# Kernel tuning notes

Measured on AMD Instinct MI355X. Metric: run time of the kernel, lower is better.

The kernel has to match this reference:

```python
import jax, jax.numpy as jnp
import numpy as np
import math

B, T, E, H = 2, 2048, 1024, 16
D = E // H  # head_dim = 64


def setup_inputs() -> dict:
    key = jax.random.key(0)
    ks = jax.random.split(key, 8)
    s = 1.0 / math.sqrt(E)
    x = jax.random.normal(ks[0], (B, T, E), dtype=jnp.float32)
    # Linear weights stored as [in, out] so y = x @ W (equivalent to torch x @ W.T)
    Wq = jax.random.normal(ks[1], (E, E), dtype=jnp.float32) * s
    Wk = jax.random.normal(ks[2], (E, E), dtype=jnp.float32) * s
    Wv = jax.random.normal(ks[3], (E, E), dtype=jnp.float32) * s
    Wa = jax.random.normal(ks[4], (E, H), dtype=jnp.float32) * s
    Wg = jax.random.normal(ks[5], (E, E), dtype=jnp.float32) * s
    Wo = jax.random.normal(ks[6], (E, E), dtype=jnp.float32) * s
    A_log = jnp.linspace(0.0, math.log(16.0), H, dtype=jnp.float32)
    dt_bias = jnp.zeros((H,), dtype=jnp.float32)
    rms_w = jnp.ones((D,), dtype=jnp.float32)
    return {"x": x, "Wq": Wq, "Wk": Wk, "Wv": Wv, "Wa": Wa, "Wg": Wg,
            "Wo": Wo, "A_log": A_log, "dt_bias": dt_bias, "rms_w": rms_w}


def _l2norm(t):
    n = jnp.linalg.norm(t, axis=-1, keepdims=True)
    return t / jnp.maximum(n, 1e-12)


def reference(x, Wq, Wk, Wv, Wa, Wg, Wo, A_log, dt_bias, rms_w):
    b, seq_len, e = x.shape
    h = A_log.shape[0]
    d = e // h
    # QKV projections, L2-normalize q and k over head_dim -> [b, h, t, d]
    q = _l2norm((x @ Wq).reshape(b, seq_len, h, d)).transpose(0, 2, 1, 3)
    k = _l2norm((x @ Wk).reshape(b, seq_len, h, d)).transpose(0, 2, 1, 3)
    v = (x @ Wv).reshape(b, seq_len, h, d).transpose(0, 2, 1, 3)
    # scalar decay alpha in (0,1]: exp(-exp(A_log) * softplus(x @ Wa + dt_bias))
    dt = jax.nn.softplus(x @ Wa + dt_bias)           # [b, t, h]
    alpha = jnp.exp(-jnp.exp(A_log) * dt)            # [b, t, h]
    # decay mask L_ij = prod_{s=j+1}^{i} alpha_s (i >= j), via cumulative log-sum
    cum_log = jnp.cumsum(jnp.log(alpha + 1e-8), axis=1).transpose(0, 2, 1)  # [b, h, t]
    log_l = cum_log[..., :, None] - cum_log[..., None, :]                   # [b, h, t, t]
    causal = jnp.tril(jnp.ones((seq_len, seq_len), dtype=bool))
    l_mat = jnp.where(causal, jnp.exp(log_l), 0.0)
    # quadratic form: Y = (L * Q K^T) V
    scores = jnp.einsum('bhid,bhjd->bhij', q, k) * l_mat
    out = jnp.einsum('bhij,bhjd->bhid', scores, v)   # [b, h, t, d]
    # RMSNorm over head_dim (eps=1e-6)
    out = out * jax.lax.rsqrt(jnp.mean(out * out, axis=-1, keepdims=True) + 1e-6) * rms_w
    out = out.transpose(0, 2, 1, 3).reshape(b, seq_len, e)
    gate = jax.nn.silu(x @ Wg)
    return (out * gate) @ Wo
```

## Files before the change

### kernel.cpp

```cpp
#include <hip/hip_runtime.h>
#include <hip/hip_bf16.h>
#include <math.h>

#define B_ 2
#define T_ 2048
#define E_ 1024
#define H_ 16
#define D_ 64
#define MTOK (B_*T_)

typedef __bf16 bf16;
typedef __bf16 bf16x8 __attribute__((ext_vector_type(8)));
typedef __bf16 bf16x4 __attribute__((ext_vector_type(4)));
typedef float  f32x4  __attribute__((ext_vector_type(4)));

__device__ __forceinline__ void gl_lds16(const void* g, void* l) {
    __builtin_amdgcn_global_load_lds(
        (const __attribute__((address_space(1))) void*)g,
        (__attribute__((address_space(3))) void*)l, 16, 0, 0);
}

__global__ void prep_weights_kernel(const float* __restrict__ Wq, const float* __restrict__ Wk,
                                    const float* __restrict__ Wv, const float* __restrict__ Wg,
                                    const float* __restrict__ Wo, const float* __restrict__ Wa,
                                    bf16* __restrict__ WTqh, bf16* __restrict__ WTql,
                                    bf16* __restrict__ WTvg, bf16* __restrict__ WTo,
                                    float* __restrict__ WaT) {
    const int tx = threadIdx.x, ty = threadIdx.y;
    if (blockIdx.x >= 5120) {
        int idx = (blockIdx.x - 5120) * 256 + ty*32 + tx;
        int h = idx >> 10, k = idx & 1023;
        WaT[idx] = Wa[k*H_ + h];
        return;
    }
    __shared__ float t[32][33];
    const int seg = blockIdx.x >> 10;
    const int bid = blockIdx.x & 1023;
    const float* src = (seg == 0) ? Wq : (seg == 1) ? Wk : (seg == 2) ? Wv
                     : (seg == 3) ? Wg : Wo;
    const int bx = bid & 31, by = bid >> 5;
#pragma unroll
    for (int i = ty; i < 32; i += 8)
        t[i][tx] = src[(size_t)(by*32 + i)*1024 + bx*32 + tx];
    __syncthreads();
    if (seg < 2) {
        bf16* dh = WTqh + (size_t)seg*1024*1024;
        bf16* dl = WTql + (size_t)seg*1024*1024;
#pragma unroll
        for (int i = ty; i < 32; i += 8) {
            float v = t[tx][i];
            bf16 h = (bf16)v;
            size_t idx = (size_t)(bx*32 + i)*1024 + by*32 + tx;
            dh[idx] = h;
            dl[idx] = (bf16)(v - (float)h);
        }
    } else {
        bf16* dst = (seg == 2) ? WTvg : (seg == 3) ? (WTvg + (size_t)1024*1024) : WTo;
#pragma unroll
        for (int i = ty; i < 32; i += 8)
            dst[(size_t)(bx*32 + i)*1024 + by*32 + tx] = (bf16)t[tx][i];
    }
}

__global__ __launch_bounds__(256) void dtx_kernel(const float* __restrict__ x,
                                                  const float* __restrict__ WaT,
                                                  const float* __restrict__ A_log,
                                                  const float* __restrict__ dt_bias,
                                                  float* __restrict__ lg,
                                                  bf16* __restrict__ xh,
                                                  bf16* __restrict__ xl) {
    __shared__ float xs[16][1032];
    const int tb = blockIdx.x * 16;
    const int tid = threadIdx.x;
#pragma unroll
    for (int v = tid; v < 2048; v += 256) {
        int row = v >> 7, c8 = (v & 127) * 8;
        const float* src = x + (size_t)(tb + row)*E_ + c8;
        float4 a = *(const float4*)src;
        float4 b = *(const float4*)(src + 4);
        float va[8] = {a.x, a.y, a.z, a.w, b.x, b.y, b.z, b.w};
        bf16x8 hv, lv;
#pragma unroll
        for (int j = 0; j < 8; ++j) {
            xs[row][c8+j] = va[j];
            bf16 h = (bf16)va[j];
            hv[j] = h;
            lv[j] = (bf16)(va[j] - (float)h);
        }
        *(bf16x8*)(xh + (size_t)(tb + row)*E_ + c8) = hv;
        *(bf16x8*)(xl + (size_t)(tb + row)*E_ + c8) = lv;
    }
    __syncthreads();
    const int i = tid >> 4, h = tid & 15;
    const float* wrow = WaT + (size_t)h*1024;
    float acc = 0.f;
#pragma unroll 8
    for (int k = 0; k < 1024; k += 4) {
        float4 xv = *(const float4*)&xs[i][k];
        float4 wv = *(const float4*)(wrow + k);
        acc += xv.x*wv.x + xv.y*wv.y + xv.z*wv.z + xv.w*wv.w;
    }
    float z   = acc + dt_bias[h];
    float dtv = (z > 20.f) ? z : log1pf(expf(z));
    float la  = -expf(A_log[h]) * dtv;
    float l   = logf(expf(la) + 1e-8f);
    int n = tb + i;
    int b = n / T_, t = n % T_;
    lg[(size_t)(b*H_ + h)*T_ + t] = l;
}

__global__ __launch_bounds__(256) void scan_kernel(const float* __restrict__ lg,
                                                   double* __restrict__ cl) {
    int row = blockIdx.x, tid = threadIdx.x;
    __shared__ double ls[256];
    const float* p = lg + (size_t)row*T_ + tid*8;
    double loc[8], s = 0.0;
#pragma unroll
    for (int j = 0; j < 8; ++j) { s += (double)p[j]; loc[j] = s; }
    ls[tid] = s;
    __syncthreads();
    for (int off = 1; off < 256; off <<= 1) {
        double add = (tid >= off) ? ls[tid - off] : 0.0;
        __syncthreads();
        ls[tid] += add;
        __syncthreads();
    }
    double prefix = ls[tid] - s;
    double* o = cl + (size_t)row*T_ + tid*8;
#pragma unroll
    for (int j = 0; j < 8; ++j) o[j] = prefix + loc[j];
}

__global__ __launch_bounds__(256, 2) void gemm_qkvg_kernel(
    const bf16* __restrict__ Ah, const bf16* __restrict__ Al,
    const bf16* __restrict__ Bh, const bf16* __restrict__ Bl,
    const bf16* __restrict__ BTvg,
    bf16* __restrict__ qhb, bf16* __restrict__ qlb,
    bf16* __restrict__ khb, bf16* __restrict__ klb,
    bf16* __restrict__ vt, float* __restrict__ Gf) {
    const int K = E_;
    __shared__ __align__(16) bf16 S[5][128*32];
    const int tid = threadIdx.x, lane = tid & 63, wid = tid >> 6;
    const int wr = wid >> 1, wc = wid & 1;
    const int lr = lane & 15, lg4 = lane >> 4;
    const int tr = tid >> 2;
    const int tc = ((tid & 3) ^ ((tid >> 3) & 3)) * 8;
    const int co = (lg4 ^ ((lr >> 1) & 3)) * 8;
    int bid = blockIdx.x;
    bid = (bid & 7) * 64 + (bid >> 3);
    const int bx = bid & 15, by = bid >> 4;
    f32x4 accq[4][4], accv[4][4];
#pragma unroll
    for (int m = 0; m < 4; ++m)
#pragma unroll
        for (int n = 0; n < 4; ++n) { accq[m][n] = (f32x4)0.0f; accv[m][n] = (f32x4)0.0f; }
    for (int k0 = 0; k0 < K; k0 += 32) {
#pragma unroll
        for (int i = 0; i < 2; ++i) {
            size_t ga = (size_t)(by*128 + i*64 + tr)*K + k0 + tc;
            size_t gb = (size_t)(bx*128 + i*64 + tr)*K + k0 + tc;
            gl_lds16(Ah   + ga, &S[0][(i*256 + wid*64)*8]);
            gl_lds16(Al   + ga, &S[1][(i*256 + wid*64)*8]);
            gl_lds16(Bh   + gb, &S[2][(i*256 + wid*64)*8]);
            gl_lds16(Bl   + gb, &S[3][(i*256 + wid*64)*8]);
            gl_lds16(BTvg + gb, &S[4][(i*256 + wid*64)*8]);
        }
        __syncthreads();
        bf16x8 ah[4], al[4], bh[4], bl[4], bv[4];
#pragma unroll
        for (int m = 0; m < 4; ++m) {
            int o = (wr*64 + m*16 + lr)*32 + co;
            ah[m] = *(const bf16x8*)&S[0][o];
            al[m] = *(const bf16x8*)&S[1][o];
        }
#pragma unroll
        for (int n = 0; n < 4; ++n) {
            int o = (wc*64 + n*16 + lr)*32 + co;
            bh[n] = *(const bf16x8*)&S[2][o];
            bl[n] = *(const bf16x8*)&S[3][o];
            bv[n] = *(const bf16x8*)&S[4][o];
        }
#pragma unroll
        for (int m = 0; m < 4; ++m)
#pragma unroll
            for (int n = 0; n < 4; ++n) {
                accq[m][n] = __builtin_amdgcn_mfma_f32_16x16x32_bf16(al[m], bh[n], accq[m][n], 0, 0, 0);
                accq[m][n] = __builtin_amdgcn_mfma_f32_16x16x32_bf16(ah[m], bl[n], accq[m][n], 0, 0, 0);
                accq[m][n] = __builtin_amdgcn_mfma_f32_16x16x32_bf16(ah[m], bh[n], accq[m][n], 0, 0, 0);
                accv[m][n] = __builtin_amdgcn_mfma_f32_16x16x32_bf16(ah[m], bv[n], accv[m][n], 0, 0, 0);
            }
        __syncthreads();
    }
    {
        const int headg = bx*2 + wc;
        bf16* dh = (headg < 16) ? qhb : khb;
        bf16* dl = (headg < 16) ? qlb : klb;
        const int h = headg & 15;
#pragma unroll
        for (int m = 0; m < 4; ++m)
#pragma unroll
            for (int r = 0; r < 4; ++r) {
                float ss = accq[m][0][r]*accq[m][0][r] + accq[m][1][r]*accq[m][1][r]
                         + accq[m][2][r]*accq[m][2][r] + accq[m][3][r]*accq[m][3][r];
#pragma unroll
                for (int off = 1; off < 16; off <<= 1) ss += __shfl_xor(ss, off, 64);
                float sc = 1.0f / fmaxf(sqrtf(ss), 1e-12f);
                int token = by*128 + wr*64 + m*16 + lg4*4 + r;
#pragma unroll
                for (int n = 0; n < 4; ++n) {
                    int d = n*16 + lr;
                    float qv = accq[m][n][r] * sc;
                    bf16 hv = (bf16)qv;
                    size_t idx = ((size_t)token*H_ + h)*64 + d;
                    dh[idx] = hv;
                    dl[idx] = (bf16)(qv - (float)hv);
                }
            }
    }
    {
        const int colbase = bx*128 + wc*64;
        const int b = by >> 4;
        if (colbase < 1024) {
            const int head = colbase >> 6;
#pragma unroll
            for (int m = 0; m < 4; ++m) {
                int trow = by*128 + wr*64 + m*16 + lg4*4;
                int tloc = trow - b*T_;
#pragma unroll
                for (int n = 0; n < 4; ++n) {
                    int d = n*16 + lr;
                    bf16x4 pk;
                    pk[0] = (bf16)accv[m][n][0]; pk[1] = (bf16)accv[m][n][1];
                    pk[2] = (bf16)accv[m][n][2]; pk[3] = (bf16)accv[m][n][3];
                    *(bf16x4*)(vt + ((size_t)((b*H_ + head)*64 + d))*T_ + tloc) = pk;
                }
            }
        } else {
#pragma unroll
            for (int m = 0; m < 4; ++m)
#pragma unroll
                for (int r = 0; r < 4; ++r) {
                    int token = by*128 + wr*64 + m*16 + lg4*4 + r;
#pragma unroll
                    for (int n = 0; n < 4; ++n) {
                        int colg = colbase - 1024 + n*16 + lr;
                        float g = accv[m][n][r];
                        Gf[(size_t)token*E_ + colg] = g / (1.0f + __expf(-g));
                    }
                }
        }
    }
}

__global__ __launch_bounds__(256) void gemm_out_kernel(
    const bf16* __restrict__ A, const bf16* __restrict__ BT, float* __restrict__ C) {
    const int K = E_, N = E_;
    __shared__ __align__(16) bf16 As[128*32];
    __shared__ __align__(16) bf16 Bs[64*32];
    int bid = blockIdx.x;
    bid = (bid & 7) * 64 + (bid >> 3);
    const int bx = bid & 15, by = bid >> 4;
    const int tid = threadIdx.x, lane = tid & 63, wid = tid >> 6;
    const int wr = wid >> 1, wc = wid & 1;
    const int lr = lane & 15, lg4 = lane >> 4;
    f32x4 acc[4][2];
#pragma unroll
    for (int m = 0; m < 4; ++m)
#pragma unroll
        for (int n = 0; n < 2; ++n) acc[m][n] = (f32x4)0.0f;
    const int tr = tid >> 2;
    const int tc = ((tid & 3) ^ ((tid >> 3) & 3)) * 8;
    const int co = (lg4 ^ ((lr >> 1) & 3)) * 8;
    for (int k0 = 0; k0 < K; k0 += 32) {
#pragma unroll
        for (int i = 0; i < 2; ++i)
            gl_lds16(A + (size_t)(by*128 + i*64 + tr)*K + k0 + tc, &As[(i*256 + wid*64)*8]);
        gl_lds16(BT + (size_t)(bx*64 + tr)*K + k0 + tc, &Bs[(wid*64)*8]);
        __syncthreads();
        bf16x8 af[4], bfr[2];
#pragma unroll
        for (int m = 0; m < 4; ++m)
            af[m] = *(const bf16x8*)&As[(wr*64 + m*16 + lr)*32 + co];
#pragma unroll
        for (int n = 0; n < 2; ++n)
            bfr[n] = *(const bf16x8*)&Bs[(wc*32 + n*16 + lr)*32 + co];
#pragma unroll
        for (int m = 0; m < 4; ++m)
#pragma unroll
            for (int n = 0; n < 2; ++n)
                acc[m][n] = __builtin_amdgcn_mfma_f32_16x16x32_bf16(af[m], bfr[n], acc[m][n], 0, 0, 0);
        __syncthreads();
    }
    const int crow = by*128 + wr*64;
    const int ccol = bx*64 + wc*32 + lr;
#pragma unroll
    for (int m = 0; m < 4; ++m)
#pragma unroll
        for (int r = 0; r < 4; ++r) {
            int row = crow + m*16 + lg4*4 + r;
#pragma unroll
            for (int n = 0; n < 2; ++n)
                C[(size_t)row*N + ccol + n*16] = acc[m][n][r];
        }
}

__global__ __launch_bounds__(256) void attn_kernel(
    const bf16* __restrict__ qh, const bf16* __restrict__ ql,
    const bf16* __restrict__ kh, const bf16* __restrict__ kl,
    const bf16* __restrict__ vt, const double* __restrict__ cl,
    const float* __restrict__ Gf, const float* __restrict__ rms_w,
    bf16* __restrict__ Y) {
    __shared__ __align__(16) bf16 Ksh[2][64*64];
    __shared__ __align__(16) bf16 Ksl[2][64*64];
    __shared__ __align__(16) bf16 Vs[2][64*64];
    __shared__ __align__(16) bf16 Ps[128*64];
    const int rank = blockIdx.x >> 5, bh = blockIdx.x & 31;
    const int it = (rank < 8) ? (15 - rank) : (rank - 8);
    const int b = bh >> 4, h = bh & 15;
    const int tid = threadIdx.x, lane = tid & 63, wid = tid >> 6;
    const int i0 = it * 128;
    const int lr = lane & 15, lg4 = lane >> 4;
    bf16x8 qfh[2][2], qfl[2][2];
#pragma unroll
    for (int mm = 0; mm < 2; ++mm) {
        int qtok = i0 + wid*32 + mm*16 + lr;
        size_t qa = (size_t)(b*T_ + qtok)*E_ + h*64 + lg4*8;
        qfh[mm][0] = *(const bf16x8*)(qh + qa);
        qfh[mm][1] = *(const bf16x8*)(qh + qa + 32);
        qfl[mm][0] = *(const bf16x8*)(ql + qa);
        qfl[mm][1] = *(const bf16x8*)(ql + qa + 32);
    }
    const double* clrow = cl + (size_t)bh*T_;
    const double base = clrow[i0];
    float cli2[2][4];
#pragma unroll
    for (int mm = 0; mm < 2; ++mm)
#pragma unroll
        for (int r = 0; r < 4; ++r)
            cli2[mm][r] = (float)(clrow[i0 + wid*32 + mm*16 + lg4*4 + r] - base);
    f32x4 oacc[2][4];
#pragma unroll
    for (int mm = 0; mm < 2; ++mm)
#pragma unroll
        for (int n = 0; n < 4; ++n) oacc[mm][n] = (f32x4)0.0f;
    const int srow8 = lane >> 3;
    const int csrc  = (lane & 7) ^ srow8;
    auto STAGE = [&](int jt, int buf) {
        const int j0 = jt * 64;
#pragma unroll
        for (int i = 0; i < 2; ++i) {
            int krow = j0 + i*32 + wid*8 + srow8;
            int drow = i*32 + wid*8 + srow8;
            size_t gk = (size_t)(b*T_ + krow)*E_ + h*64 + csrc*8;
            gl_lds16(kh + gk, &Ksh[buf][(i*32 + wid*8)*64]);
            gl_lds16(kl + gk, &Ksl[buf][(i*32 + wid*8)*64]);
            gl_lds16(vt + (size_t)(bh*64 + drow)*T_ + j0 + csrc*8, &Vs[buf][(i*32 + wid*8)*64]);
        }
    };
    const int niter = 2*it + 2;
    int jt_min;
    {
        int lo = 0, hi = niter - 1;
        while (lo < hi) {
            int mid = (lo + hi) >> 1;
            int jend = mid*64 + 63; if (jend > i0) jend = i0;
            if (clrow[jend] <= base + 95.0) hi = mid; else lo = mid + 1;
        }
        jt_min = lo;
    }
    STAGE(jt_min, 0);
    __syncthreads();
    int cur = 0;
    for (int jt = jt_min; jt < niter; ++jt) {
        const int j0 = jt * 64;
        if (jt + 1 < niter) STAGE(jt + 1, cur ^ 1);
#pragma unroll
        for (int n = 0; n < 4; ++n) {
            const int r = n*16 + lr;
            const int sw = r & 7;
            const int ko = r*64;
            bf16x8 k_h0 = *(const bf16x8*)&Ksh[cur][ko + ((lg4 ^ sw)*8)];
            bf16x8 k_h1 = *(const bf16x8*)&Ksh[cur][ko + (((lg4+4) ^ sw)*8)];
            bf16x8 k_l0 = *(const bf16x8*)&Ksl[cur][ko + ((lg4 ^ sw)*8)];
            bf16x8 k_l1 = *(const bf16x8*)&Ksl[cur][ko + (((lg4+4) ^ sw)*8)];
            const int j = j0 + r;
            const float cj = (float)(clrow[j] - base);
#pragma unroll
            for (int mm = 0; mm < 2; ++mm) {
                f32x4 s = (f32x4)0.0f;
                __builtin_amdgcn_s_setprio(1);
                s = __builtin_amdgcn_mfma_f32_16x16x32_bf16(qfl[mm][0], k_h0, s, 0, 0, 0);
                s = __builtin_amdgcn_mfma_f32_16x16x32_bf16(qfl[mm][1], k_h1, s, 0, 0, 0);
                s = __builtin_amdgcn_mfma_f32_16x16x32_bf16(qfh[mm][0], k_l0, s, 0, 0, 0);
                s = __builtin_amdgcn_mfma_f32_16x16x32_bf16(qfh[mm][1], k_l1, s, 0, 0, 0);
                s = __builtin_amdgcn_mfma_f32_16x16x32_bf16(qfh[mm][0], k_h0, s, 0, 0, 0);
                s = __builtin_amdgcn_mfma_f32_16x16x32_bf16(qfh[mm][1], k_h1, s, 0, 0, 0);
                __builtin_amdgcn_s_setprio(0);
                const int prbase = wid*32 + mm*16 + lg4*4;
#pragma unroll
                for (int r4 = 0; r4 < 4; ++r4) {
                    const int pr = prbase + r4;
                    const int qrow = i0 + pr;
                    float val = (j <= qrow)
                        ? s[r4] * __expf(cli2[mm][r4] - cj) : 0.0f;
                    const int cw = n*2 + (lr >> 3);
                    Ps[pr*64 + ((cw ^ (pr & 7))*8) + (lane & 7)] = (bf16)val;
                }
            }
        }
#pragma unroll
        for (int kk = 0; kk < 2; ++kk) {
            const int js = kk*4 + lg4;
            bf16x8 pf[2];
#pragma unroll
            for (int mm = 0; mm < 2; ++mm) {
                const int rp = wid*32 + mm*16 + lr;
                pf[mm] = *(const bf16x8*)&Ps[rp*64 + ((js ^ (rp & 7))*8)];
            }
            __builtin_amdgcn_s_setprio(1);
#pragma unroll
            for (int n = 0; n < 4; ++n) {
                const int rv = n*16 + lr;
                bf16x8 vf = *(const bf16x8*)&Vs[cur][rv*64 + ((js ^ (rv & 7))*8)];
                oacc[0][n] = __builtin_amdgcn_mfma_f32_16x16x32_bf16(pf[0], vf, oacc[0][n], 0, 0, 0);
                oacc[1][n] = __builtin_amdgcn_mfma_f32_16x16x32_bf16(pf[1], vf, oacc[1][n], 0, 0, 0);
            }
            __builtin_amdgcn_s_setprio(0);
        }
        __syncthreads();
        cur ^= 1;
    }
#pragma unroll
    for (int mm = 0; mm < 2; ++mm)
#pragma unroll
        for (int r = 0; r < 4; ++r) {
            float ss = oacc[mm][0][r]*oacc[mm][0][r] + oacc[mm][1][r]*oacc[mm][1][r]
                     + oacc[mm][2][r]*oacc[mm][2][r] + oacc[mm][3][r]*oacc[mm][3][r];
#pragma unroll
            for (int off = 1; off < 16; off <<= 1) ss += __shfl_xor(ss, off, 64);
            const float scale = rsqrtf(ss * (1.0f/64.0f) + 1e-6f);
            const int gtok = b*T_ + i0 + wid*32 + mm*16 + lg4*4 + r;
#pragma unroll
            for (int n = 0; n < 4; ++n) {
                const int d = n*16 + lr;
                float o = oacc[mm][n][r] * scale * rms_w[d];
                float gate = Gf[(size_t)gtok*E_ + h*64 + d];
                Y[(size_t)gtok*E_ + h*64 + d] = (bf16)(o * gate);
            }
        }
}

extern "C" void kernel_launch(void* const* d_in, const int* in_sizes, int n_in,
                              void* d_out, int out_size, void* d_ws, size_t ws_size,
                              hipStream_t stream) {
    const float* x       = (const float*)d_in[0];
    const float* Wq      = (const float*)d_in[1];
    const float* Wk      = (const float*)d_in[2];
    const float* Wv      = (const float*)d_in[3];
    const float* Wa      = (const float*)d_in[4];
    const float* Wg      = (const float*)d_in[5];
    const float* Wo      = (const float*)d_in[6];
    const float* A_log   = (const float*)d_in[7];
    const float* dt_bias = (const float*)d_in[8];
    const float* rms_w   = (const float*)d_in[9];
    float* out = (float*)d_out;

    char* w = (char*)d_ws;
    size_t off = 0;
    auto alloc = [&](size_t bytes) {
        void* p = w + off; off += (bytes + 255) & ~(size_t)255; return p;
    };
    bf16*   xh   = (bf16*)  alloc((size_t)MTOK*E_*2);
    bf16*   xl   = (bf16*)  alloc((size_t)MTOK*E_*2);
    bf16*   WTqh = (bf16*)  alloc((size_t)2048*E_*2);
    bf16*   WTql = (bf16*)  alloc((size_t)2048*E_*2);
    bf16*   WTvg = (bf16*)  alloc((size_t)2048*E_*2);
    bf16*   WTo  = (bf16*)  alloc((size_t)E_*E_*2);
    bf16*   qhb  = (bf16*)  alloc((size_t)MTOK*E_*2);
    bf16*   qlb  = (bf16*)  alloc((size_t)MTOK*E_*2);
    bf16*   khb  = (bf16*)  alloc((size_t)MTOK*E_*2);
    bf16*   klb  = (bf16*)  alloc((size_t)MTOK*E_*2);
    bf16*   vt   = (bf16*)  alloc((size_t)MTOK*E_*2);
    float*  Gf   = (float*) alloc((size_t)MTOK*E_*4);
    float*  lg   = (float*) alloc((size_t)B_*H_*T_*4);
    double* cl   = (double*)alloc((size_t)B_*H_*T_*8);
    bf16*   Yb   = (bf16*)  alloc((size_t)MTOK*E_*2);
    float*  WaT  = (float*) alloc((size_t)H_*E_*4);

    hipLaunchKernelGGL(prep_weights_kernel, dim3(5184), dim3(32, 8), 0, stream,
                       Wq, Wk, Wv, Wg, Wo, Wa, WTqh, WTql, WTvg, WTo, WaT);

    hipLaunchKernelGGL(dtx_kernel, dim3(256), dim3(256), 0, stream,
                       x, WaT, A_log, dt_bias, lg, xh, xl);
    hipLaunchKernelGGL(scan_kernel, dim3(B_*H_), dim3(256), 0, stream, lg, cl);

    hipLaunchKernelGGL(gemm_qkvg_kernel, dim3(512), dim3(256), 0, stream,
                       xh, xl, WTqh, WTql, WTvg, qhb, qlb, khb, klb, vt, Gf);

    hipLaunchKernelGGL(attn_kernel, dim3(512), dim3(256), 0, stream,
                       qhb, qlb, khb, klb, vt, cl, Gf, rms_w, Yb);

    hipLaunchKernelGGL(gemm_out_kernel, dim3(512), dim3(256), 0, stream, Yb, WTo, out);
}
```

Before: 159.2 us.

## Double-buffer LDS staging in projection GEMMs and remap qkvg block-to-XCD tiling

Both the fused QKV/gate GEMM and the output GEMM now keep two LDS buffers and issue the global-to-LDS loads for the next k-slice before computing on the current one, so load latency can overlap with MFMA work. The qkvg kernel drops its minimum-two-blocks occupancy hint and changes how block ids map to tiles so each XCD handles adjacent column tiles. The cost is doubled LDS use, about 80 KB per block in the qkvg kernel, which may cut occupancy to one block per CU. The single barrier per iteration relies on async LDS loads finishing by that barrier, which the hardware's wait-before-barrier behaviour should provide.

```diff
diff --git a/kernel.cpp b/kernel.cpp
--- a/kernel.cpp
+++ b/kernel.cpp
@@ -131,7 +131,7 @@
     for (int j = 0; j < 8; ++j) o[j] = prefix + loc[j];
 }
 
-__global__ __launch_bounds__(256, 2) void gemm_qkvg_kernel(
+__global__ __launch_bounds__(256) void gemm_qkvg_kernel(
     const bf16* __restrict__ Ah, const bf16* __restrict__ Al,
     const bf16* __restrict__ Bh, const bf16* __restrict__ Bl,
     const bf16* __restrict__ BTvg,
@@ -139,46 +139,50 @@
     bf16* __restrict__ khb, bf16* __restrict__ klb,
     bf16* __restrict__ vt, float* __restrict__ Gf) {
     const int K = E_;
-    __shared__ __align__(16) bf16 S[5][128*32];
+    __shared__ __align__(16) bf16 S[2][5][128*32];
     const int tid = threadIdx.x, lane = tid & 63, wid = tid >> 6;
     const int wr = wid >> 1, wc = wid & 1;
     const int lr = lane & 15, lg4 = lane >> 4;
     const int tr = tid >> 2;
     const int tc = ((tid & 3) ^ ((tid >> 3) & 3)) * 8;
     const int co = (lg4 ^ ((lr >> 1) & 3)) * 8;
-    int bid = blockIdx.x;
-    bid = (bid & 7) * 64 + (bid >> 3);
-    const int bx = bid & 15, by = bid >> 4;
+    const int xcd = blockIdx.x & 7, wk = blockIdx.x >> 3;
+    const int bx = xcd*2 + (wk & 1), by = wk >> 1;
     f32x4 accq[4][4], accv[4][4];
 #pragma unroll
     for (int m = 0; m < 4; ++m)
 #pragma unroll
         for (int n = 0; n < 4; ++n) { accq[m][n] = (f32x4)0.0f; accv[m][n] = (f32x4)0.0f; }
-    for (int k0 = 0; k0 < K; k0 += 32) {
+    auto STAGE = [&](int k0, int buf) {
 #pragma unroll
         for (int i = 0; i < 2; ++i) {
             size_t ga = (size_t)(by*128 + i*64 + tr)*K + k0 + tc;
             size_t gb = (size_t)(bx*128 + i*64 + tr)*K + k0 + tc;
-            gl_lds16(Ah   + ga, &S[0][(i*256 + wid*64)*8]);
-            gl_lds16(Al   + ga, &S[1][(i*256 + wid*64)*8]);
-            gl_lds16(Bh   + gb, &S[2][(i*256 + wid*64)*8]);
-            gl_lds16(Bl   + gb, &S[3][(i*256 + wid*64)*8]);
-            gl_lds16(BTvg + gb, &S[4][(i*256 + wid*64)*8]);
-        }
-        __syncthreads();
+            gl_lds16(Ah   + ga, &S[buf][0][(i*256 + wid*64)*8]);
+            gl_lds16(Al   + ga, &S[buf][1][(i*256 + wid*64)*8]);
+            gl_lds16(Bh   + gb, &S[buf][2][(i*256 + wid*64)*8]);
+            gl_lds16(Bl   + gb, &S[buf][3][(i*256 + wid*64)*8]);
+            gl_lds16(BTvg + gb, &S[buf][4][(i*256 + wid*64)*8]);
+        }
+    };
+    STAGE(0, 0);
+    __syncthreads();
+    int cur = 0;
+    for (int k0 = 0; k0 < K; k0 += 32) {
+        if (k0 + 32 < K) STAGE(k0 + 32, cur ^ 1);
         bf16x8 ah[4], al[4], bh[4], bl[4], bv[4];
 #pragma unroll
         for (int m = 0; m < 4; ++m) {
             int o = (wr*64 + m*16 + lr)*32 + co;
-            ah[m] = *(const bf16x8*)&S[0][o];
-            al[m] = *(const bf16x8*)&S[1][o];
+            ah[m] = *(const bf16x8*)&S[cur][0][o];
+            al[m] = *(const bf16x8*)&S[cur][1][o];
         }
 #pragma unroll
         for (int n = 0; n < 4; ++n) {
             int o = (wc*64 + n*16 + lr)*32 + co;
-            bh[n] = *(const bf16x8*)&S[2][o];
-            bl[n] = *(const bf16x8*)&S[3][o];
-            bv[n] = *(const bf16x8*)&S[4][o];
+            bh[n] = *(const bf16x8*)&S[cur][2][o];
+            bl[n] = *(const bf16x8*)&S[cur][3][o];
+            bv[n] = *(const bf16x8*)&S[cur][4][o];
         }
 #pragma unroll
         for (int m = 0; m < 4; ++m)
@@ -190,6 +194,7 @@
                 accv[m][n] = __builtin_amdgcn_mfma_f32_16x16x32_bf16(ah[m], bv[n], accv[m][n], 0, 0, 0);
             }
         __syncthreads();
+        cur ^= 1;
     }
     {
         const int headg = bx*2 + wc;
@@ -255,8 +260,8 @@
 __global__ __launch_bounds__(256) void gemm_out_kernel(
     const bf16* __restrict__ A, const bf16* __restrict__ BT, float* __restrict__ C) {
     const int K = E_, N = E_;
-    __shared__ __align__(16) bf16 As[128*32];
-    __shared__ __align__(16) bf16 Bs[64*32];
+    __shared__ __align__(16) bf16 As[2][128*32];
+    __shared__ __align__(16) bf16 Bs[2][64*32];
     int bid = blockIdx.x;
     bid = (bid & 7) * 64 + (bid >> 3);
     const int bx = bid & 15, by = bid >> 4;
@@ -271,25 +276,31 @@
     const int tr = tid >> 2;
     const int tc = ((tid & 3) ^ ((tid >> 3) & 3)) * 8;
     const int co = (lg4 ^ ((lr >> 1) & 3)) * 8;
+    auto STAGE = [&](int k0, int buf) {
+#pragma unroll
+        for (int i = 0; i < 2; ++i)
+            gl_lds16(A + (size_t)(by*128 + i*64 + tr)*K + k0 + tc, &As[buf][(i*256 + wid*64)*8]);
+        gl_lds16(BT + (size_t)(bx*64 + tr)*K + k0 + tc, &Bs[buf][(wid*64)*8]);
+    };
+    STAGE(0, 0);
+    __syncthreads();
+    int cur = 0;
     for (int k0 = 0; k0 < K; k0 += 32) {
-#pragma unroll
-        for (int i = 0; i < 2; ++i)
-            gl_lds16(A + (size_t)(by*128 + i*64 + tr)*K + k0 + tc, &As[(i*256 + wid*64)*8]);
-        gl_lds16(BT + (size_t)(bx*64 + tr)*K + k0 + tc, &Bs[(wid*64)*8]);
-        __syncthreads();
+        if (k0 + 32 < K) STAGE(k0 + 32, cur ^ 1);
         bf16x8 af[4], bfr[2];
 #pragma unroll
         for (int m = 0; m < 4; ++m)
-            af[m] = *(const bf16x8*)&As[(wr*64 + m*16 + lr)*32 + co];
+            af[m] = *(const bf16x8*)&As[cur][(wr*64 + m*16 + lr)*32 + co];
 #pragma unroll
         for (int n = 0; n < 2; ++n)
-            bfr[n] = *(const bf16x8*)&Bs[(wc*32 + n*16 + lr)*32 + co];
+            bfr[n] = *(const bf16x8*)&Bs[cur][(wc*32 + n*16 + lr)*32 + co];
 #pragma unroll
         for (int m = 0; m < 4; ++m)
 #pragma unroll
             for (int n = 0; n < 2; ++n)
                 acc[m][n] = __builtin_amdgcn_mfma_f32_16x16x32_bf16(af[m], bfr[n], acc[m][n], 0, 0, 0);
         __syncthreads();
+        cur ^= 1;
     }
     const int crow = by*128 + wr*64;
     const int ccol = bx*64 + wc*32 + lr;
```

Measured after the change: 197.6 us. 24.1% more time.
